# Optimization experiments

Measured on AMD Instinct MI355X. Metric: run time of the kernel, lower is better.

The kernel has to match this reference:

```python
import jax, jax.numpy as jnp
import numpy as np

B, T, C, H = 4, 2048, 768, 12
D = C // H


def setup_inputs() -> dict:
    key = jax.random.key(0)
    ks = jax.random.split(key, 7)
    s = 0.02
    return {
        "q": jax.random.normal(ks[0], (B, T, C), jnp.float32),
        "k": jax.random.normal(ks[1], (B, T, C), jnp.float32),
        "v": jax.random.normal(ks[2], (B, T, C), jnp.float32),
        "w_q": jax.random.normal(ks[3], (C, C), jnp.float32) * s,
        "w_k": jax.random.normal(ks[4], (C, C), jnp.float32) * s,
        "w_v": jax.random.normal(ks[5], (C, C), jnp.float32) * s,
        "w_o": jax.random.normal(ks[6], (C, C), jnp.float32) * s,
    }


def reference(q, k, v, w_q, w_k, w_v, w_o):
    # Linear projections (torch Linear: x @ W^T, bias=False)
    qh = (q @ w_q.T).reshape(B, T, H, D).transpose(0, 2, 1, 3)  # [B,H,T,D]
    kh = (k @ w_k.T).reshape(B, T, H, D).transpose(0, 2, 1, 3)
    vh = (v @ w_v.T).reshape(B, T, H, D).transpose(0, 2, 1, 3)
    scale = 1.0 / jnp.sqrt(jnp.asarray(D, qh.dtype))
    att = jnp.einsum("bhqd,bhkd->bhqk", qh, kh) * scale  # [B,H,T,T]
    causal = jnp.tril(jnp.ones((T, T), bool))
    att = jnp.where(causal[None, None], att, -jnp.inf)
    att = jax.nn.softmax(att, axis=-1)
    y = jnp.einsum("bhqk,bhkd->bhqd", att, vh)  # [B,H,T,D]
    y = y.transpose(0, 2, 1, 3).reshape(B, T, C)
    return y @ w_o.T
```

## Files before the change

kernel.cpp:

```cpp
#include <hip/hip_runtime.h>

#define BB 4
#define TT 2048
#define CC 768
#define HH 12
#define DD 64
#define MM (BB * TT)

#define QSCALE 0.18033688011112042f

typedef __attribute__((ext_vector_type(8))) __bf16 bf16x8;
typedef __attribute__((ext_vector_type(4))) __bf16 bf16x4;
typedef __attribute__((ext_vector_type(4))) float f32x4;

__device__ inline void gload16(const void* g, void* l) {
  __builtin_amdgcn_global_load_lds(
      (const __attribute__((address_space(1))) unsigned int*)g,
      (__attribute__((address_space(3))) unsigned int*)l, 16, 0, 0);
}

__device__ inline void cast_body(const float* __restrict__ s, __bf16* __restrict__ d) {
  long i = ((long)blockIdx.x * 256 + threadIdx.x) * 8;
  f32x4 a = *(const f32x4*)(s + i);
  f32x4 b = *(const f32x4*)(s + i + 4);
  bf16x8 o;
  o[0] = (__bf16)a[0]; o[1] = (__bf16)a[1]; o[2] = (__bf16)a[2]; o[3] = (__bf16)a[3];
  o[4] = (__bf16)b[0]; o[5] = (__bf16)b[1]; o[6] = (__bf16)b[2]; o[7] = (__bf16)b[3];
  *(bf16x8*)(d + i) = o;
}

__global__ __launch_bounds__(256) void cast3(const float* __restrict__ s0, const float* __restrict__ s1,
                                             const float* __restrict__ s2,
                                             __bf16* d0, __bf16* d1, __bf16* d2) {
  const float* s = blockIdx.y == 0 ? s0 : blockIdx.y == 1 ? s1 : s2;
  __bf16* d = blockIdx.y == 0 ? d0 : blockIdx.y == 1 ? d1 : d2;
  cast_body(s, d);
}

__global__ __launch_bounds__(256) void cast4(const float* __restrict__ s0, const float* __restrict__ s1,
                                             const float* __restrict__ s2, const float* __restrict__ s3,
                                             __bf16* d0, __bf16* d1, __bf16* d2, __bf16* d3) {
  const float* s; __bf16* d;
  switch (blockIdx.y) {
    case 0: s = s0; d = d0; break;
    case 1: s = s1; d = d1; break;
    case 2: s = s2; d = d2; break;
    default: s = s3; d = d3; break;
  }
  cast_body(s, d);
}

__device__ inline void stage_tile(const __bf16* __restrict__ A, const __bf16* __restrict__ W,
                                  long m0, long n0, int k0,
                                  __bf16* As, __bf16* Bs, int wave, int lane) {
#pragma unroll
  for (int i = 0; i < 4; ++i) {
    const int r = wave + i * 4;
    const int L = r * 1024 + lane * 16;
    const int row = L >> 7;
    const int sc = (L >> 4) & 7;
    const int gc = sc ^ (row & 7);
    gload16(A + (m0 + row) * CC + k0 + gc * 8, As + r * 512);
    gload16(W + (n0 + row) * CC + k0 + gc * 8, Bs + r * 512);
  }
}

__device__ inline void compute_tile(const __bf16* As, const __bf16* Bs, f32x4 (&acc)[4][4],
                                    int wr, int wc, int l15, int g) {
#pragma unroll
  for (int kk = 0; kk < 2; ++kk) {
    bf16x8 af[4], bfr[4];
#pragma unroll
    for (int mi = 0; mi < 4; ++mi) {
      const int row = wr + mi * 16 + l15;
      const int c = (kk * 4 + g) ^ (row & 7);
      af[mi] = *(const bf16x8*)&As[row * 64 + c * 8];
    }
#pragma unroll
    for (int ni = 0; ni < 4; ++ni) {
      const int row = wc + ni * 16 + l15;
      const int c = (kk * 4 + g) ^ (row & 7);
      bfr[ni] = *(const bf16x8*)&Bs[row * 64 + c * 8];
    }
#pragma unroll
    for (int mi = 0; mi < 4; ++mi)
#pragma unroll
      for (int ni = 0; ni < 4; ++ni)
        acc[mi][ni] = __builtin_amdgcn_mfma_f32_16x16x32_bf16(af[mi], bfr[ni], acc[mi][ni], 0, 0, 0);
  }
}

template <int MODE>
__global__ __launch_bounds__(256) void gemm_proj(
    const __bf16* __restrict__ A0, const __bf16* __restrict__ A1, const __bf16* __restrict__ A2,
    const __bf16* __restrict__ W0, const __bf16* __restrict__ W1, const __bf16* __restrict__ W2,
    void* D0, void* D1, void* D2) {
  __shared__ __align__(16) char smem[65536];
  __bf16* As0 = (__bf16*)smem;
  __bf16* Bs0 = (__bf16*)(smem + 16384);
  __bf16* As1 = (__bf16*)(smem + 32768);
  __bf16* Bs1 = (__bf16*)(smem + 49152);

  const int z = blockIdx.z;
  const __bf16* __restrict__ A = z == 0 ? A0 : z == 1 ? A1 : A2;
  const __bf16* __restrict__ W = z == 0 ? W0 : z == 1 ? W1 : W2;
  const long m0 = blockIdx.y * 128;
  const long n0 = blockIdx.x * 128;
  const int tid = threadIdx.x;
  const int wave = tid >> 6, lane = tid & 63;
  const int l15 = lane & 15, g = lane >> 4;
  const int wr = (wave >> 1) * 64, wc = (wave & 1) * 64;

  f32x4 acc[4][4] = {};

  stage_tile(A, W, m0, n0, 0, As0, Bs0, wave, lane);
  __syncthreads();
  for (int kt = 0; kt < 12; kt += 2) {
    stage_tile(A, W, m0, n0, (kt + 1) * 64, As1, Bs1, wave, lane);
    compute_tile(As0, Bs0, acc, wr, wc, l15, g);
    __syncthreads();
    if (kt + 2 < 12) stage_tile(A, W, m0, n0, (kt + 2) * 64, As0, Bs0, wave, lane);
    compute_tile(As1, Bs1, acc, wr, wc, l15, g);
    __syncthreads();
  }

  const int b = (int)(m0 >> 11);
  const int t0 = (int)(m0 & (TT - 1));
  if (MODE == 1) {
    float* Ef = (float*)smem;
    float* Dst = (float*)D0;
    for (int p = 0; p < 2; ++p) {
      if (p) __syncthreads();
      if ((wr >> 6) == p) {
#pragma unroll
        for (int mi = 0; mi < 4; ++mi)
#pragma unroll
          for (int ni = 0; ni < 4; ++ni)
#pragma unroll
            for (int j = 0; j < 4; ++j) {
              const int ml = mi * 16 + g * 4 + j;
              const int n = wc + ni * 16 + l15;
              *(float*)((char*)Ef + ml * 512 + ((n * 4) ^ (((ml >> 2) & 7) << 4))) = acc[mi][ni][j];
            }
      }
      __syncthreads();
#pragma unroll
      for (int sw = 0; sw < 8; ++sw) {
        const int r = sw * 8 + (tid >> 5);
        const int c = (tid & 31) * 4;
        f32x4 vv = *(const f32x4*)((char*)Ef + r * 512 + ((c * 4) ^ (((r >> 2) & 7) << 4)));
        *(f32x4*)&Dst[(m0 + p * 64 + r) * CC + n0 + c] = vv;
      }
    }
  } else {
    __bf16* Eh = (__bf16*)smem;
    __bf16* Dst = (__bf16*)(z == 0 ? D0 : z == 1 ? D1 : D2);
    for (int p = 0; p < 2; ++p) {
      if (p) __syncthreads();
      if (z != 2) {
        if ((wr >> 6) == p) {
#pragma unroll
          for (int mi = 0; mi < 4; ++mi)
#pragma unroll
            for (int ni = 0; ni < 4; ++ni)
#pragma unroll
              for (int j = 0; j < 4; ++j) {
                const int ml = mi * 16 + g * 4 + j;
                const int n = wc + ni * 16 + l15;
                float v = acc[mi][ni][j];
                if (z == 0) v *= QSCALE;
                *(__bf16*)((char*)Eh + ml * 256 + ((n * 2) ^ (((ml >> 2) & 7) << 4))) = (__bf16)v;
              }
        }
      } else {
        if ((wc >> 6) == p) {
#pragma unroll
          for (int mi = 0; mi < 4; ++mi)
#pragma unroll
            for (int ni = 0; ni < 4; ++ni)
#pragma unroll
              for (int j = 0; j < 4; ++j) {
                const int nl = ni * 16 + l15;
                const int mm = wr + mi * 16 + g * 4 + j;
                *(__bf16*)((char*)Eh + nl * 256 + ((mm * 2) ^ ((nl & 7) << 4))) = (__bf16)acc[mi][ni][j];
              }
        }
      }
      __syncthreads();
#pragma unroll
      for (int sw = 0; sw < 4; ++sw) {
        const int r = sw * 16 + (tid >> 4);
        const int c = (tid & 15) * 8;
        if (z != 2) {
          bf16x8 vv = *(const bf16x8*)((char*)Eh + r * 256 + ((c * 2) ^ (((r >> 2) & 7) << 4)));
          const int t = t0 + p * 64 + r;
          const int n = (int)n0 + c;
          const int h = n >> 6, d = n & 63;
          *(bf16x8*)&Dst[(((long)(b * HH + h)) * TT + t) * DD + d] = vv;
        } else {
          bf16x8 vv = *(const bf16x8*)((char*)Eh + r * 256 + ((c * 2) ^ ((r & 7) << 4)));
          const int n = (int)n0 + p * 64 + r;
          const int h = n >> 6, d = n & 63;
          *(bf16x8*)&Dst[(((long)(b * HH + h)) * DD + d) * TT + t0 + c] = vv;
        }
      }
    }
  }
}

__global__ __launch_bounds__(256) void attn_fwd(
    const __bf16* __restrict__ Qh, const __bf16* __restrict__ Kh,
    const __bf16* __restrict__ Vh, __bf16* __restrict__ Y) {
  __shared__ __bf16 Kl[2][64 * 64];
  __shared__ __bf16 Vl[2][64 * 64];
  __shared__ __bf16 Pl[4][16 * 64];

  const int bh = blockIdx.y;
  const int a = blockIdx.x;
  const int tid = threadIdx.x, wave = tid >> 6, lane = tid & 63;
  const int l15 = lane & 15, g = lane >> 4;
  const __bf16* Kbase = Kh + (long)bh * TT * DD;
  const __bf16* VTbase = Vh + (long)bh * DD * TT;
  const int b = bh / HH, h = bh % HH;
  char* Pb = (char*)&Pl[wave][0];

  const int s_a = a + 1;
  const int total = 33;

  int qt = a;
  int qrow = qt * 64 + wave * 16 + l15;
  bf16x8 qf0, qf1;
  {
    const __bf16* qptr = Qh + ((long)bh * TT + qrow) * DD;
    qf0 = *(const bf16x8*)(qptr + g * 8);
    qf1 = *(const bf16x8*)(qptr + 32 + g * 8);
  }

  f32x4 oacc[4] = {};
  float m = -1e30f, lsum = 0.f;

#pragma unroll
  for (int i = 0; i < 2; ++i) {
    const int r = wave + i * 4;
    const int L = r * 1024 + lane * 16;
    const int row = L >> 7, sc = (L >> 4) & 7, gc = sc ^ (row & 7);
    gload16(Kbase + (long)row * DD + gc * 8, &Kl[0][r * 512]);
    gload16(VTbase + (long)row * TT + gc * 8, &Vl[0][r * 512]);
  }

  for (int s = 0; s < total; ++s) {
    __syncthreads();

    if (s + 1 < total) {
      const int kt1 = (s + 1 >= s_a) ? (s + 1 - s_a) : (s + 1);
      const int kv1 = kt1 * 64;
      __bf16* Kd = Kl[(s + 1) & 1];
      __bf16* Vd = Vl[(s + 1) & 1];
#pragma unroll
      for (int i = 0; i < 2; ++i) {
        const int r = wave + i * 4;
        const int L = r * 1024 + lane * 16;
        const int row = L >> 7, sc = (L >> 4) & 7, gc = sc ^ (row & 7);
        gload16(Kbase + (long)(kv1 + row) * DD + gc * 8, Kd + r * 512);
        gload16(VTbase + (long)row * TT + kv1 + gc * 8, Vd + r * 512);
      }
    }

    if (s == s_a) {
      float lrow = lsum + __shfl_xor(lsum, 16);
      lrow += __shfl_xor(lrow, 32);
#pragma unroll
      for (int j = 0; j < 4; ++j) {
        const float inv = 1.0f / __shfl(lrow, g * 4 + j);
        const int q = qt * 64 + wave * 16 + g * 4 + j;
#pragma unroll
        for (int ni = 0; ni < 4; ++ni)
          Y[((long)(b * TT + q)) * CC + h * DD + ni * 16 + l15] = (__bf16)(oacc[ni][j] * inv);
      }
      qt = 31 - a;
      qrow = qt * 64 + wave * 16 + l15;
      const __bf16* qptr = Qh + ((long)bh * TT + qrow) * DD;
      qf0 = *(const bf16x8*)(qptr + g * 8);
      qf1 = *(const bf16x8*)(qptr + 32 + g * 8);
#pragma unroll
      for (int ni = 0; ni < 4; ++ni) oacc[ni] = (f32x4){0.f, 0.f, 0.f, 0.f};
      m = -1e30f; lsum = 0.f;
    }

    const int kt = (s >= s_a) ? (s - s_a) : s;
    const int kv0 = kt * 64;
    const bool maskt = (kt == qt);
    const __bf16* Kc = Kl[s & 1];
    const __bf16* Vc = Vl[s & 1];

    f32x4 sacc[4] = {};
#pragma unroll
    for (int mi = 0; mi < 4; ++mi) {
      const int row = mi * 16 + l15;
      const int c0 = g ^ (row & 7);
      const int c1 = (4 + g) ^ (row & 7);
      bf16x8 kfa = *(const bf16x8*)&Kc[row * 64 + c0 * 8];
      bf16x8 kfb = *(const bf16x8*)&Kc[row * 64 + c1 * 8];
      sacc[mi] = __builtin_amdgcn_mfma_f32_16x16x32_bf16(kfa, qf0, sacc[mi], 0, 0, 0);
      sacc[mi] = __builtin_amdgcn_mfma_f32_16x16x32_bf16(kfb, qf1, sacc[mi], 0, 0, 0);
    }

    float ps[4][4];
    float tmax = -3e30f;
    if (maskt) {
#pragma unroll
      for (int mi = 0; mi < 4; ++mi)
#pragma unroll
        for (int j = 0; j < 4; ++j) {
          float sv = sacc[mi][j];
          const int kv = kv0 + mi * 16 + g * 4 + j;
          if (kv > qrow) sv = -3e30f;
          ps[mi][j] = sv;
          tmax = fmaxf(tmax, sv);
        }
    } else {
#pragma unroll
      for (int mi = 0; mi < 4; ++mi)
#pragma unroll
        for (int j = 0; j < 4; ++j) {
          const float sv = sacc[mi][j];
          ps[mi][j] = sv;
          tmax = fmaxf(tmax, sv);
        }
    }

    if (!__all(tmax <= m + 8.0f)) {
      float full = fmaxf(tmax, __shfl_xor(tmax, 16));
      full = fmaxf(full, __shfl_xor(full, 32));
      const float mnew = fmaxf(m, full);
      const float corr = exp2f(m - mnew);
#pragma unroll
      for (int j = 0; j < 4; ++j) {
        const float cj = __shfl(corr, g * 4 + j);
#pragma unroll
        for (int ni = 0; ni < 4; ++ni) oacc[ni][j] *= cj;
      }
      lsum *= corr;
      m = mnew;
    }

#pragma unroll
    for (int mi = 0; mi < 4; ++mi) {
      bf16x4 pv;
#pragma unroll
      for (int j = 0; j < 4; ++j) {
        const float p = exp2f(ps[mi][j] - m);
        lsum += p;
        pv[j] = (__bf16)p;
      }
      *(bf16x4*)(Pb + l15 * 128 + ((mi * 32 + g * 8) ^ ((l15 & 7) << 4))) = pv;
    }

#pragma unroll
    for (int ks = 0; ks < 2; ++ks) {
      bf16x8 pa = *(const bf16x8*)(Pb + l15 * 128 + ((ks * 64 + g * 16) ^ ((l15 & 7) << 4)));
#pragma unroll
      for (int ni = 0; ni < 4; ++ni) {
        const int d = ni * 16 + l15;
        const int c = (ks * 4 + g) ^ (d & 7);
        bf16x8 vf = *(const bf16x8*)&Vc[d * 64 + c * 8];
        oacc[ni] = __builtin_amdgcn_mfma_f32_16x16x32_bf16(pa, vf, oacc[ni], 0, 0, 0);
      }
    }
  }

  {
    float lrow = lsum + __shfl_xor(lsum, 16);
    lrow += __shfl_xor(lrow, 32);
#pragma unroll
    for (int j = 0; j < 4; ++j) {
      const float inv = 1.0f / __shfl(lrow, g * 4 + j);
      const int q = qt * 64 + wave * 16 + g * 4 + j;
#pragma unroll
      for (int ni = 0; ni < 4; ++ni)
        Y[((long)(b * TT + q)) * CC + h * DD + ni * 16 + l15] = (__bf16)(oacc[ni][j] * inv);
    }
  }
}

extern "C" void kernel_launch(void* const* d_in, const int* in_sizes, int n_in,
                              void* d_out, int out_size, void* d_ws, size_t ws_size,
                              hipStream_t stream) {
  (void)in_sizes; (void)n_in; (void)out_size; (void)ws_size;
  const float* q  = (const float*)d_in[0];
  const float* k  = (const float*)d_in[1];
  const float* v  = (const float*)d_in[2];
  const float* wq = (const float*)d_in[3];
  const float* wk = (const float*)d_in[4];
  const float* wv = (const float*)d_in[5];
  const float* wo = (const float*)d_in[6];

  char* ws = (char*)d_ws;
  const long SZX = (long)MM * CC * 2;
  const long SZW = (long)CC * CC * 2;
  __bf16* xq  = (__bf16*)(ws);
  __bf16* xk  = (__bf16*)(ws + SZX);
  __bf16* xv  = (__bf16*)(ws + 2 * SZX);
  __bf16* wwq = (__bf16*)(ws + 3 * SZX);
  __bf16* wwk = (__bf16*)(ws + 3 * SZX + SZW);
  __bf16* wwv = (__bf16*)(ws + 3 * SZX + 2 * SZW);
  __bf16* wwo = (__bf16*)(ws + 3 * SZX + 3 * SZW);
  __bf16* qh  = (__bf16*)(ws + 3 * SZX + 4 * SZW);
  __bf16* kh  = (__bf16*)(ws + 4 * SZX + 4 * SZW);
  __bf16* vh  = (__bf16*)(ws + 5 * SZX + 4 * SZW);
  __bf16* y   = xq;

  cast3<<<dim3((MM * CC) / 2048, 3, 1), 256, 0, stream>>>(q, k, v, xq, xk, xv);
  cast4<<<dim3((CC * CC) / 2048, 4, 1), 256, 0, stream>>>(wq, wk, wv, wo, wwq, wwk, wwv, wwo);
  gemm_proj<0><<<dim3(CC / 128, MM / 128, 3), 256, 0, stream>>>(xq, xk, xv, wwq, wwk, wwv, qh, kh, vh);
  attn_fwd<<<dim3(TT / 128, BB * HH, 1), 256, 0, stream>>>(qh, kh, vh, y);
  gemm_proj<1><<<dim3(CC / 128, MM / 128, 1), 256, 0, stream>>>(y, y, y, wwo, wwo, wwo, d_out, d_out, d_out);
}
```

Measured before the change: 261.9 us.

## Remap block IDs for XCD-local L2 reuse, add MFMA priority hints, use native exp2

```diff
diff --git a/kernel.cpp b/kernel.cpp
--- a/kernel.cpp
+++ b/kernel.cpp
@@ -82,11 +82,13 @@
       const int c = (kk * 4 + g) ^ (row & 7);
       bfr[ni] = *(const bf16x8*)&Bs[row * 64 + c * 8];
     }
+    __builtin_amdgcn_s_setprio(1);
 #pragma unroll
     for (int mi = 0; mi < 4; ++mi)
 #pragma unroll
       for (int ni = 0; ni < 4; ++ni)
         acc[mi][ni] = __builtin_amdgcn_mfma_f32_16x16x32_bf16(af[mi], bfr[ni], acc[mi][ni], 0, 0, 0);
+    __builtin_amdgcn_s_setprio(0);
   }
 }
 
@@ -101,11 +103,17 @@
   __bf16* As1 = (__bf16*)(smem + 32768);
   __bf16* Bs1 = (__bf16*)(smem + 49152);
 
-  const int z = blockIdx.z;
+  const int id = blockIdx.x;
+  const int xcd = id & 7, slot = id >> 3;
+  const int n_idx = slot % 6;
+  const int mzg = xcd + 8 * (slot / 6);
+  const int z = (MODE == 0) ? (mzg >> 6) : 0;
+  const int m_idx = (MODE == 0) ? (mzg & 63) : mzg;
+
   const __bf16* __restrict__ A = z == 0 ? A0 : z == 1 ? A1 : A2;
   const __bf16* __restrict__ W = z == 0 ? W0 : z == 1 ? W1 : W2;
-  const long m0 = blockIdx.y * 128;
-  const long n0 = blockIdx.x * 128;
+  const long m0 = (long)m_idx * 128;
+  const long n0 = (long)n_idx * 128;
   const int tid = threadIdx.x;
   const int wave = tid >> 6, lane = tid & 63;
   const int l15 = lane & 15, g = lane >> 4;
@@ -215,8 +223,11 @@
   __shared__ __bf16 Vl[2][64 * 64];
   __shared__ __bf16 Pl[4][16 * 64];
 
-  const int bh = blockIdx.y;
-  const int a = blockIdx.x;
+  const int id = blockIdx.x;
+  const int xcd = id & 7, slot = id >> 3;
+  const int a = slot & 15;
+  const int bh = xcd + 8 * (slot >> 4);
+
   const int tid = threadIdx.x, wave = tid >> 6, lane = tid & 63;
   const int l15 = lane & 15, g = lane >> 4;
   const __bf16* Kbase = Kh + (long)bh * TT * DD;
@@ -294,6 +305,7 @@
     const __bf16* Vc = Vl[s & 1];
 
     f32x4 sacc[4] = {};
+    __builtin_amdgcn_s_setprio(1);
 #pragma unroll
     for (int mi = 0; mi < 4; ++mi) {
       const int row = mi * 16 + l15;
@@ -304,6 +316,7 @@
       sacc[mi] = __builtin_amdgcn_mfma_f32_16x16x32_bf16(kfa, qf0, sacc[mi], 0, 0, 0);
       sacc[mi] = __builtin_amdgcn_mfma_f32_16x16x32_bf16(kfb, qf1, sacc[mi], 0, 0, 0);
     }
+    __builtin_amdgcn_s_setprio(0);
 
     float ps[4][4];
     float tmax = -3e30f;
@@ -333,7 +346,7 @@
       float full = fmaxf(tmax, __shfl_xor(tmax, 16));
       full = fmaxf(full, __shfl_xor(full, 32));
       const float mnew = fmaxf(m, full);
-      const float corr = exp2f(m - mnew);
+      const float corr = __builtin_amdgcn_exp2f(m - mnew);
 #pragma unroll
       for (int j = 0; j < 4; ++j) {
         const float cj = __shfl(corr, g * 4 + j);
@@ -349,13 +362,14 @@
       bf16x4 pv;
 #pragma unroll
       for (int j = 0; j < 4; ++j) {
-        const float p = exp2f(ps[mi][j] - m);
+        const float p = __builtin_amdgcn_exp2f(ps[mi][j] - m);
         lsum += p;
         pv[j] = (__bf16)p;
       }
       *(bf16x4*)(Pb + l15 * 128 + ((mi * 32 + g * 8) ^ ((l15 & 7) << 4))) = pv;
     }
 
+    __builtin_amdgcn_s_setprio(1);
 #pragma unroll
     for (int ks = 0; ks < 2; ++ks) {
       bf16x8 pa = *(const bf16x8*)(Pb + l15 * 128 + ((ks * 64 + g * 16) ^ ((l15 & 7) << 4)));
@@ -367,6 +381,7 @@
         oacc[ni] = __builtin_amdgcn_mfma_f32_16x16x32_bf16(pa, vf, oacc[ni], 0, 0, 0);
       }
     }
+    __builtin_amdgcn_s_setprio(0);
   }
 
   {
@@ -412,7 +427,7 @@
 
   cast3<<<dim3((MM * CC) / 2048, 3, 1), 256, 0, stream>>>(q, k, v, xq, xk, xv);
   cast4<<<dim3((CC * CC) / 2048, 4, 1), 256, 0, stream>>>(wq, wk, wv, wo, wwq, wwk, wwv, wwo);
-  gemm_proj<0><<<dim3(CC / 128, MM / 128, 3), 256, 0, stream>>>(xq, xk, xv, wwq, wwk, wwv, qh, kh, vh);
-  attn_fwd<<<dim3(TT / 128, BB * HH, 1), 256, 0, stream>>>(qh, kh, vh, y);
-  gemm_proj<1><<<dim3(CC / 128, MM / 128, 1), 256, 0, stream>>>(y, y, y, wwo, wwo, wwo, d_out, d_out, d_out);
-}
+  gemm_proj<0><<<dim3(1152, 1, 1), 256, 0, stream>>>(xq, xk, xv, wwq, wwk, wwv, qh, kh, vh);
+  attn_fwd<<<dim3(768, 1, 1), 256, 0, stream>>>(qh, kh, vh, y);
+  gemm_proj<1><<<dim3(384, 1, 1), 256, 0, stream>>>(y, y, y, wwo, wwo, wwo, d_out, d_out, d_out);
+}
```

Result: faster. 240.7 us (-8.1%).
